# Performance work log

Measured on AMD Instinct MI355X. Metric: run time of the kernel, lower is better.

The kernel has to match this reference:

```python
import jax, jax.numpy as jnp
import numpy as np

N, M, D_IN, HID = 6144, 6144, 16, 256
TEMP = 0.1


def setup_inputs() -> dict:
    key = jax.random.key(0)
    ks = jax.random.split(key, 6)
    sc = lambda k, shape, s: jax.random.normal(k, shape, jnp.float32) * s
    return {
        "q_multivectors": jax.random.normal(ks[0], (N, D_IN), jnp.float32),
        "ret_multivectors": jax.random.normal(ks[1], (M, D_IN), jnp.float32),
        # compressor: LazyLinear(D_IN->HID), GELU, Linear(HID->HID)
        "W1": sc(ks[2], (HID, D_IN), 0.1), "b1": jnp.zeros((HID,), jnp.float32),
        "W2": sc(ks[3], (HID, HID), 0.05), "b2": jnp.zeros((HID,), jnp.float32),
        # nn.Bilinear(HID, HID, 1): weight [1,HID,HID] -> [HID,HID], bias [1] -> scalar
        "Wb": sc(ks[4], (HID, HID), 0.02), "b_bil": jnp.zeros((), jnp.float32),
        "slack_q": jnp.zeros((1,), jnp.float32),
        "slack_ret": jnp.zeros((1,), jnp.float32),
    }


def reference(q_multivectors, ret_multivectors, W1, b1, W2, b2, Wb, b_bil, slack_q, slack_ret):
    def compress(x):  # Linear -> exact GELU -> Linear
        return jax.nn.gelu(x @ W1.T + b1, approximate=False) @ W2.T + b2

    h_q = compress(q_multivectors)    # [n, H]
    h_r = compress(ret_multivectors)  # [m, H]

    # Bilinear(h_q_i, h_r_j) as low-rank factorization: (h_q @ Wb) @ h_r^T + bias
    logits = (h_q @ Wb) @ h_r.T + b_bil  # [n, m]
    n, m = logits.shape

    # row softmax with slack column, then drop slack
    with_slack_col = jnp.concatenate([logits, jnp.broadcast_to(slack_q, (n, 1))], axis=1)
    pi_rows = jax.nn.softmax(with_slack_col / TEMP, axis=1)[:, :-1]

    # column softmax with slack row, then drop slack
    with_slack_row = jnp.concatenate([logits, jnp.broadcast_to(slack_ret, (1, m))], axis=0)
    pi_cols = jax.nn.softmax(with_slack_row / TEMP, axis=0)[:-1, :]

    pi_approx = 0.5 * (pi_rows + pi_cols)
    return pi_approx, logits
```

## Files before the change

### kernel.cpp

```cpp
#include <hip/hip_runtime.h>
#include <hip/hip_bf16.h>
#include <math.h>

#define NQ 6144
#define MR 6144
#define DIN 16
#define HID 256
#define INV_T 10.0f

typedef __attribute__((ext_vector_type(4))) float f32x4;
typedef __attribute__((ext_vector_type(8))) short bf16x8;


static __device__ __forceinline__ unsigned short f2bf(float f) {
  __hip_bfloat16 h = __float2bfloat16(f);
  return __builtin_bit_cast(unsigned short, h);
}

static __device__ __forceinline__ void gload16(const void* g, void* l) {
  __builtin_amdgcn_global_load_lds(
      (const __attribute__((address_space(1))) unsigned int*)g,
      (__attribute__((address_space(3))) unsigned int*)l, 16, 0, 0);
}

__global__ __launch_bounds__(256) void k_prep(
    const float* __restrict__ W2, const float* __restrict__ Wb,
    unsigned short* __restrict__ W2bf, unsigned short* __restrict__ Wbt)
{
  const int idx = blockIdx.x * 256 + threadIdx.x;
  W2bf[idx] = f2bf(W2[idx]);
  const int j = idx >> 8, c = idx & 255;
  Wbt[(size_t)c * 256 + j] = f2bf(Wb[idx]);
}

__global__ __launch_bounds__(256) void k_compress(
    const float* __restrict__ q, const float* __restrict__ ret,
    const float* __restrict__ W1, const float* __restrict__ b1,
    const unsigned short* __restrict__ W2bf, const float* __restrict__ b2,
    const unsigned short* __restrict__ Wbt,
    unsigned short* __restrict__ Apk, unsigned short* __restrict__ Bpk)
{
  const int tid = threadIdx.x;
  const bool is_q = blockIdx.x < (NQ / 16);
  const int grp = is_q ? blockIdx.x : blockIdx.x - NQ / 16;
  const int row0 = grp * 16;
  const float* x = is_q ? q : ret;

  __shared__ float xs[16][DIN];
  __shared__ __align__(16) unsigned short tb[16 * 256];
  __shared__ __align__(16) unsigned short hb[16 * 256];

  ((float*)xs)[tid] = x[(size_t)row0 * DIN + tid];
  __syncthreads();

  {
    float w[DIN];
#pragma unroll
    for (int d = 0; d < DIN; ++d) w[d] = W1[tid * DIN + d];
    const float bb = b1[tid];
#pragma unroll
    for (int rr = 0; rr < 16; ++rr) {
      float a = bb;
#pragma unroll
      for (int d = 0; d < DIN; ++d) a += xs[rr][d] * w[d];
      a = 0.5f * a * (1.0f + erff(a * 0.70710678118654752f));
      tb[rr * 256 + (tid ^ ((rr & 7) << 3))] = f2bf(a);
    }
  }
  __syncthreads();

  const int wid = tid >> 6, lane = tid & 63;
  const int l15 = lane & 15;
  const int lk = (lane >> 4) * 8;

  {
    f32x4 acc[4];
#pragma unroll
    for (int ci = 0; ci < 4; ++ci) acc[ci] = (f32x4)0.0f;

    for (int kk = 0; kk < HID; kk += 32) {
      const bf16x8 a = *(const bf16x8*)&tb[l15 * 256 + ((kk + lk) ^ ((l15 & 7) << 3))];
#pragma unroll
      for (int ci = 0; ci < 4; ++ci) {
        const int bc = wid * 64 + ci * 16 + l15;
        const bf16x8 b = *(const bf16x8*)&W2bf[(size_t)bc * HID + kk + lk];
        acc[ci] = __builtin_amdgcn_mfma_f32_16x16x32_bf16(a, b, acc[ci], 0, 0, 0);
      }
    }

#pragma unroll
    for (int ci = 0; ci < 4; ++ci) {
      const int col = wid * 64 + ci * 16 + l15;
      const float bb2 = b2[col];
#pragma unroll
      for (int qq = 0; qq < 4; ++qq) {
        const int row = (lane >> 4) * 4 + qq;
        hb[row * 256 + (col ^ ((row & 7) << 3))] = f2bf(acc[ci][qq] + bb2);
      }
    }
  }
  __syncthreads();

  if (!is_q) {
#pragma unroll
    for (int i = 0; i < 2; ++i) {
      const int u = i * 256 + tid;
      const int kc = u >> 6, lr = (u >> 2) & 15, ks = u & 3;
      const int k = kc * 32 + ks * 8;
      const bf16x8 v = *(const bf16x8*)&hb[lr * 256 + (k ^ ((lr & 7) << 3))];
      *(bf16x8*)&Bpk[(size_t)grp * 4096 + (size_t)u * 8] = v;
    }
    return;
  }

  {
    f32x4 acc[4];
#pragma unroll
    for (int ci = 0; ci < 4; ++ci) acc[ci] = (f32x4)0.0f;

    for (int kk = 0; kk < HID; kk += 32) {
      const bf16x8 a = *(const bf16x8*)&hb[l15 * 256 + ((kk + lk) ^ ((l15 & 7) << 3))];
#pragma unroll
      for (int ci = 0; ci < 4; ++ci) {
        const int bc = wid * 64 + ci * 16 + l15;
        const bf16x8 b = *(const bf16x8*)&Wbt[(size_t)bc * HID + kk + lk];
        acc[ci] = __builtin_amdgcn_mfma_f32_16x16x32_bf16(a, b, acc[ci], 0, 0, 0);
      }
    }

#pragma unroll
    for (int ci = 0; ci < 4; ++ci) {
      const int col = wid * 64 + ci * 16 + l15;
#pragma unroll
      for (int qq = 0; qq < 4; ++qq) {
        const int row = (lane >> 4) * 4 + qq;
        tb[row * 256 + (col ^ ((row & 7) << 3))] = f2bf(acc[ci][qq]);
      }
    }
  }
  __syncthreads();

#pragma unroll
  for (int i = 0; i < 2; ++i) {
    const int u = i * 256 + tid;
    const int kc = u >> 6, lr = (u >> 2) & 15, ks = u & 3;
    const int k = kc * 32 + ks * 8;
    const bf16x8 v = *(const bf16x8*)&tb[lr * 256 + (k ^ ((lr & 7) << 3))];
    *(bf16x8*)&Apk[(size_t)grp * 4096 + (size_t)u * 8] = v;
  }
}

__global__ __launch_bounds__(512, 4) void k_gemm(
    const unsigned short* __restrict__ Apk,
    const unsigned short* __restrict__ Bpk,
    const float* __restrict__ b_bil,
    float* __restrict__ logF,
    float* __restrict__ rowPS,
    float* __restrict__ colPS)
{
  const int tid = threadIdx.x;
  const int wid = tid >> 6, lane = tid & 63;
  const int wr = wid >> 1, wc = wid & 1;

  const int orig = blockIdx.y * 48 + blockIdx.x;
  const int nid = (orig & 7) * 144 + (orig >> 3);
  const int brow = (nid / 48) * 256;
  const int bcol = (nid % 48) * 128;
  const int brow16 = brow >> 4, bcol16 = bcol >> 4;

  __shared__ __align__(16) unsigned short As[2][8192];
  __shared__ __align__(16) unsigned short Bs[2][4096];

  const int l15 = lane & 15;
  const int ksg = lane >> 4;

  f32x4 acc[4][4];
#pragma unroll
  for (int i = 0; i < 4; ++i)
#pragma unroll
    for (int j = 0; j < 4; ++j) acc[i][j] = (f32x4)0.0f;

  gload16(Apk + (size_t)(brow16 + 2 * wid) * 4096 + lane * 8,
          &As[0][(2 * wid) * 512]);
  gload16(Apk + (size_t)(brow16 + 2 * wid + 1) * 4096 + lane * 8,
          &As[0][(2 * wid + 1) * 512]);
  gload16(Bpk + (size_t)(bcol16 + wid) * 4096 + lane * 8, &Bs[0][wid * 512]);

  int cur = 0;
  for (int kc = 0; kc < 8; ++kc) {
    __syncthreads();
    if (kc < 7) {
      const int kn = (kc + 1) * 512;
      gload16(Apk + (size_t)(brow16 + 2 * wid) * 4096 + kn + lane * 8,
              &As[cur ^ 1][(2 * wid) * 512]);
      gload16(Apk + (size_t)(brow16 + 2 * wid + 1) * 4096 + kn + lane * 8,
              &As[cur ^ 1][(2 * wid + 1) * 512]);
      gload16(Bpk + (size_t)(bcol16 + wid) * 4096 + kn + lane * 8,
              &Bs[cur ^ 1][wid * 512]);
    }
    const int fo = l15 * 32 + ksg * 8;
    bf16x8 a[4], b[4];
#pragma unroll
    for (int mi = 0; mi < 4; ++mi)
      a[mi] = *(const bf16x8*)&As[cur][(wr * 4 + mi) * 512 + fo];
#pragma unroll
    for (int ni = 0; ni < 4; ++ni)
      b[ni] = *(const bf16x8*)&Bs[cur][(wc * 4 + ni) * 512 + fo];
#pragma unroll
    for (int mi = 0; mi < 4; ++mi)
#pragma unroll
      for (int ni = 0; ni < 4; ++ni)
        acc[mi][ni] = __builtin_amdgcn_mfma_f32_16x16x32_bf16(
            a[mi], b[ni], acc[mi][ni], 0, 0, 0);
    cur ^= 1;
  }

  const float bb = b_bil[0];
#pragma unroll
  for (int mi = 0; mi < 4; ++mi)
#pragma unroll
    for (int ni = 0; ni < 4; ++ni)
#pragma unroll
      for (int qq = 0; qq < 4; ++qq) acc[mi][ni][qq] += bb;

  const int r0 = brow + wr * 64 + ksg * 4;
  const int c0 = bcol + wc * 64 + l15;
#pragma unroll
  for (int mi = 0; mi < 4; ++mi)
#pragma unroll
    for (int qq = 0; qq < 4; ++qq) {
      const int rr = r0 + mi * 16 + qq;
#pragma unroll
      for (int ni = 0; ni < 4; ++ni)
        __builtin_nontemporal_store(acc[mi][ni][qq],
                                    &logF[(size_t)rr * MR + c0 + ni * 16]);
    }

  const int cb = (bcol >> 6) + wc;
  const int rb = (brow >> 6) + wr;
  float csum[4] = {0.0f, 0.0f, 0.0f, 0.0f};
#pragma unroll
  for (int mi = 0; mi < 4; ++mi) {
#pragma unroll
    for (int qq = 0; qq < 4; ++qq) {
      float rsum = 0.0f;
#pragma unroll
      for (int ni = 0; ni < 4; ++ni) {
        const float e = __expf(acc[mi][ni][qq] * INV_T);
        rsum += e;
        csum[ni] += e;
      }
      rsum += __shfl_xor(rsum, 1);
      rsum += __shfl_xor(rsum, 2);
      rsum += __shfl_xor(rsum, 4);
      rsum += __shfl_xor(rsum, 8);
      if (l15 == 0) rowPS[(size_t)cb * NQ + (r0 + mi * 16 + qq)] = rsum;
    }
  }
#pragma unroll
  for (int ni = 0; ni < 4; ++ni) {
    csum[ni] += __shfl_xor(csum[ni], 16);
    csum[ni] += __shfl_xor(csum[ni], 32);
  }
  if (lane < 16) {
#pragma unroll
    for (int ni = 0; ni < 4; ++ni)
      colPS[(size_t)rb * MR + (bcol + wc * 64 + ni * 16 + lane)] = csum[ni];
  }
}

__global__ __launch_bounds__(256) void k_comb(
    const float* __restrict__ rowPS, const float* __restrict__ colPS,
    const float* __restrict__ slack_q, const float* __restrict__ slack_ret,
    float* __restrict__ rowR, float* __restrict__ colR)
{
  const int idx = blockIdx.x * 256 + threadIdx.x;
  const bool is_row = idx < NQ;
  const int i = is_row ? idx : idx - NQ;
  const float* ps = is_row ? rowPS : colPS;

  float s = 0.0f;
  for (int c = 0; c < 96; ++c) s += ps[(size_t)c * NQ + i];
  s += __expf((is_row ? slack_q[0] : slack_ret[0]) * INV_T);

  if (is_row) rowR[i] = 0.5f / s;
  else        colR[i] = 0.5f / s;
}

__global__ __launch_bounds__(256) void k_final(
    const float* __restrict__ logF,
    const float* __restrict__ rowR, const float* __restrict__ colR,
    float* __restrict__ out_pi)
{
  const int row = blockIdx.x / 6;
  const int seg = blockIdx.x % 6;
  const int col = seg * 1024 + threadIdx.x * 4;
  const size_t base = (size_t)row * MR + col;

  const float rinv = rowR[row];
  const f32x4 cv = *(const f32x4*)(colR + col);
  const f32x4 l4 = *(const f32x4*)(logF + base);

  f32x4 o;
  o.x = __expf(l4.x * INV_T) * (rinv + cv.x);
  o.y = __expf(l4.y * INV_T) * (rinv + cv.y);
  o.z = __expf(l4.z * INV_T) * (rinv + cv.z);
  o.w = __expf(l4.w * INV_T) * (rinv + cv.w);
  __builtin_nontemporal_store(o, (f32x4*)(out_pi + base));
}

extern "C" void kernel_launch(void* const* d_in, const int* in_sizes, int n_in,
                              void* d_out, int out_size, void* d_ws, size_t ws_size,
                              hipStream_t stream) {
  const float* q  = (const float*)d_in[0];
  const float* r  = (const float*)d_in[1];
  const float* W1 = (const float*)d_in[2];
  const float* b1 = (const float*)d_in[3];
  const float* W2 = (const float*)d_in[4];
  const float* b2 = (const float*)d_in[5];
  const float* Wb = (const float*)d_in[6];
  const float* bb = (const float*)d_in[7];
  const float* sq = (const float*)d_in[8];
  const float* sr = (const float*)d_in[9];

  float* out_pi = (float*)d_out;
  float* out_lg = out_pi + (size_t)NQ * MR;

  char* w = (char*)d_ws;
  size_t off = 0;
  auto alloc = [&](size_t bytes) {
    void* p = w + off;
    off += (bytes + 255) & ~(size_t)255;
    return p;
  };
  unsigned short* Apk  = (unsigned short*)alloc((size_t)NQ * HID * 2);
  unsigned short* Bpk  = (unsigned short*)alloc((size_t)MR * HID * 2);
  unsigned short* W2bf = (unsigned short*)alloc((size_t)HID * HID * 2);
  unsigned short* Wbt  = (unsigned short*)alloc((size_t)HID * HID * 2);
  float* rowR = (float*)alloc((size_t)NQ * 4);
  float* colR = (float*)alloc((size_t)MR * 4);

  float* rowPS = out_pi + (size_t)0 * 96 * NQ;
  float* colPS = out_pi + (size_t)1 * 96 * NQ;

  k_prep<<<dim3(HID * HID / 256), 256, 0, stream>>>(W2, Wb, W2bf, Wbt);
  k_compress<<<dim3((NQ + MR) / 16), 256, 0, stream>>>(q, r, W1, b1, W2bf, b2,
                                                       Wbt, Apk, Bpk);
  k_gemm<<<dim3(48, 24), 512, 0, stream>>>(Apk, Bpk, bb, out_lg, rowPS, colPS);
  k_comb<<<dim3((NQ + MR) / 256), 256, 0, stream>>>(
      rowPS, colPS, sq, sr, rowR, colR);
  k_final<<<dim3(NQ * 6), 256, 0, stream>>>(out_lg, rowR, colR, out_pi);
}
```

Before: 143.9 us.

## Store bf16 exp values from GEMM and triple-buffer the K loop

The GEMM epilogue now also writes exp(logit/T) as bf16 into a workspace buffer when the workspace is large enough. The final kernel then reads 2-byte values instead of re-reading fp32 logits and recomputing exp, which cuts its read traffic in half. The GEMM main loop also moves from double to triple buffering with explicit vmcnt waits and raw barriers, to overlap loads more deeply. The trade-offs are an extra 75 MB write in the GEMM, more LDS per block, and bf16 rounding of the exp values, which lowers the precision of pi.

Result: slower. 154.0 us (+7.0%).

```diff
diff --git a/kernel.cpp b/kernel.cpp
--- a/kernel.cpp
+++ b/kernel.cpp
@@ -15,6 +15,10 @@
 static __device__ __forceinline__ unsigned short f2bf(float f) {
   __hip_bfloat16 h = __float2bfloat16(f);
   return __builtin_bit_cast(unsigned short, h);
+}
+static __device__ __forceinline__ float bf2f(unsigned short u) {
+  unsigned int x = ((unsigned int)u) << 16;
+  return __builtin_bit_cast(float, x);
 }
 
 static __device__ __forceinline__ void gload16(const void* g, void* l) {
@@ -150,13 +154,15 @@
   }
 }
 
+template <bool WRITE_E>
 __global__ __launch_bounds__(512, 4) void k_gemm(
     const unsigned short* __restrict__ Apk,
     const unsigned short* __restrict__ Bpk,
     const float* __restrict__ b_bil,
     float* __restrict__ logF,
     float* __restrict__ rowPS,
-    float* __restrict__ colPS)
+    float* __restrict__ colPS,
+    unsigned short* __restrict__ Ebuf)
 {
   const int tid = threadIdx.x;
   const int wid = tid >> 6, lane = tid & 63;
@@ -168,8 +174,8 @@
   const int bcol = (nid % 48) * 128;
   const int brow16 = brow >> 4, bcol16 = bcol >> 4;
 
-  __shared__ __align__(16) unsigned short As[2][8192];
-  __shared__ __align__(16) unsigned short Bs[2][4096];
+  __shared__ __align__(16) unsigned short As[3][8192];
+  __shared__ __align__(16) unsigned short Bs[3][4096];
 
   const int l15 = lane & 15;
   const int ksg = lane >> 4;
@@ -180,39 +186,49 @@
 #pragma unroll
     for (int j = 0; j < 4; ++j) acc[i][j] = (f32x4)0.0f;
 
-  gload16(Apk + (size_t)(brow16 + 2 * wid) * 4096 + lane * 8,
-          &As[0][(2 * wid) * 512]);
-  gload16(Apk + (size_t)(brow16 + 2 * wid + 1) * 4096 + lane * 8,
-          &As[0][(2 * wid + 1) * 512]);
-  gload16(Bpk + (size_t)(bcol16 + wid) * 4096 + lane * 8, &Bs[0][wid * 512]);
-
-  int cur = 0;
+  const unsigned short* a0 = Apk + (size_t)(brow16 + 2 * wid) * 4096 + lane * 8;
+  const unsigned short* a1 = a0 + 4096;
+  const unsigned short* b0 = Bpk + (size_t)(bcol16 + wid) * 4096 + lane * 8;
+
+  gload16(a0, &As[0][(2 * wid) * 512]);
+  gload16(a1, &As[0][(2 * wid + 1) * 512]);
+  gload16(b0, &Bs[0][wid * 512]);
+  gload16(a0 + 512, &As[1][(2 * wid) * 512]);
+  gload16(a1 + 512, &As[1][(2 * wid + 1) * 512]);
+  gload16(b0 + 512, &Bs[1][wid * 512]);
+
   for (int kc = 0; kc < 8; ++kc) {
-    __syncthreads();
-    if (kc < 7) {
-      const int kn = (kc + 1) * 512;
-      gload16(Apk + (size_t)(brow16 + 2 * wid) * 4096 + kn + lane * 8,
-              &As[cur ^ 1][(2 * wid) * 512]);
-      gload16(Apk + (size_t)(brow16 + 2 * wid + 1) * 4096 + kn + lane * 8,
-              &As[cur ^ 1][(2 * wid + 1) * 512]);
-      gload16(Bpk + (size_t)(bcol16 + wid) * 4096 + kn + lane * 8,
-              &Bs[cur ^ 1][wid * 512]);
-    }
+    if (kc < 6) {
+      const int kn = (kc + 2) * 512;
+      const int nb = (kc + 2) % 3;
+      gload16(a0 + kn, &As[nb][(2 * wid) * 512]);
+      gload16(a1 + kn, &As[nb][(2 * wid + 1) * 512]);
+      gload16(b0 + kn, &Bs[nb][wid * 512]);
+      asm volatile("s_waitcnt vmcnt(6)" ::: "memory");
+    } else if (kc == 6) {
+      asm volatile("s_waitcnt vmcnt(3)" ::: "memory");
+    } else {
+      asm volatile("s_waitcnt vmcnt(0)" ::: "memory");
+    }
+    __builtin_amdgcn_s_barrier();
+
+    const int cb3 = kc % 3;
     const int fo = l15 * 32 + ksg * 8;
     bf16x8 a[4], b[4];
 #pragma unroll
     for (int mi = 0; mi < 4; ++mi)
-      a[mi] = *(const bf16x8*)&As[cur][(wr * 4 + mi) * 512 + fo];
+      a[mi] = *(const bf16x8*)&As[cb3][(wr * 4 + mi) * 512 + fo];
 #pragma unroll
     for (int ni = 0; ni < 4; ++ni)
-      b[ni] = *(const bf16x8*)&Bs[cur][(wc * 4 + ni) * 512 + fo];
+      b[ni] = *(const bf16x8*)&Bs[cb3][(wc * 4 + ni) * 512 + fo];
 #pragma unroll
     for (int mi = 0; mi < 4; ++mi)
 #pragma unroll
       for (int ni = 0; ni < 4; ++ni)
         acc[mi][ni] = __builtin_amdgcn_mfma_f32_16x16x32_bf16(
             a[mi], b[ni], acc[mi][ni], 0, 0, 0);
-    cur ^= 1;
+
+    __builtin_amdgcn_s_barrier();
   }
 
   const float bb = b_bil[0];
@@ -243,10 +259,14 @@
   for (int mi = 0; mi < 4; ++mi) {
 #pragma unroll
     for (int qq = 0; qq < 4; ++qq) {
+      const int rr = r0 + mi * 16 + qq;
       float rsum = 0.0f;
 #pragma unroll
       for (int ni = 0; ni < 4; ++ni) {
         const float e = __expf(acc[mi][ni][qq] * INV_T);
+        if (WRITE_E)
+          __builtin_nontemporal_store(
+              f2bf(e), &Ebuf[(size_t)rr * MR + c0 + ni * 16]);
         rsum += e;
         csum[ni] += e;
       }
@@ -254,7 +274,7 @@
       rsum += __shfl_xor(rsum, 2);
       rsum += __shfl_xor(rsum, 4);
       rsum += __shfl_xor(rsum, 8);
-      if (l15 == 0) rowPS[(size_t)cb * NQ + (r0 + mi * 16 + qq)] = rsum;
+      if (l15 == 0) rowPS[(size_t)cb * NQ + rr] = rsum;
     }
   }
 #pragma unroll
@@ -285,6 +305,34 @@
 
   if (is_row) rowR[i] = 0.5f / s;
   else        colR[i] = 0.5f / s;
+}
+
+__global__ __launch_bounds__(256) void k_final_e(
+    const unsigned short* __restrict__ Ebuf,
+    const float* __restrict__ rowR, const float* __restrict__ colR,
+    float* __restrict__ out_pi)
+{
+  const int row = blockIdx.x / 3;
+  const int seg = blockIdx.x % 3;
+  const int col = seg * 2048 + threadIdx.x * 8;
+  const size_t base = (size_t)row * MR + col;
+
+  const float rinv = rowR[row];
+  const bf16x8 e8 = *(const bf16x8*)(Ebuf + base);
+  const f32x4 cv0 = *(const f32x4*)(colR + col);
+  const f32x4 cv1 = *(const f32x4*)(colR + col + 4);
+
+  f32x4 o0, o1;
+  o0.x = bf2f((unsigned short)e8[0]) * (rinv + cv0.x);
+  o0.y = bf2f((unsigned short)e8[1]) * (rinv + cv0.y);
+  o0.z = bf2f((unsigned short)e8[2]) * (rinv + cv0.z);
+  o0.w = bf2f((unsigned short)e8[3]) * (rinv + cv0.w);
+  o1.x = bf2f((unsigned short)e8[4]) * (rinv + cv1.x);
+  o1.y = bf2f((unsigned short)e8[5]) * (rinv + cv1.y);
+  o1.z = bf2f((unsigned short)e8[6]) * (rinv + cv1.z);
+  o1.w = bf2f((unsigned short)e8[7]) * (rinv + cv1.w);
+  __builtin_nontemporal_store(o0, (f32x4*)(out_pi + base));
+  __builtin_nontemporal_store(o1, (f32x4*)(out_pi + base + 4));
 }
 
 __global__ __launch_bounds__(256) void k_final(
@@ -340,14 +388,27 @@
   float* rowR = (float*)alloc((size_t)NQ * 4);
   float* colR = (float*)alloc((size_t)MR * 4);
 
+  unsigned short* Ebuf = nullptr;
+  if (ws_size >= off + (size_t)NQ * MR * 2 + 1024)
+    Ebuf = (unsigned short*)alloc((size_t)NQ * MR * 2);
+
   float* rowPS = out_pi + (size_t)0 * 96 * NQ;
   float* colPS = out_pi + (size_t)1 * 96 * NQ;
 
   k_prep<<<dim3(HID * HID / 256), 256, 0, stream>>>(W2, Wb, W2bf, Wbt);
   k_compress<<<dim3((NQ + MR) / 16), 256, 0, stream>>>(q, r, W1, b1, W2bf, b2,
                                                        Wbt, Apk, Bpk);
-  k_gemm<<<dim3(48, 24), 512, 0, stream>>>(Apk, Bpk, bb, out_lg, rowPS, colPS);
-  k_comb<<<dim3((NQ + MR) / 256), 256, 0, stream>>>(
-      rowPS, colPS, sq, sr, rowR, colR);
-  k_final<<<dim3(NQ * 6), 256, 0, stream>>>(out_lg, rowR, colR, out_pi);
-}
+  if (Ebuf) {
+    k_gemm<true><<<dim3(48, 24), 512, 0, stream>>>(
+        Apk, Bpk, bb, out_lg, rowPS, colPS, Ebuf);
+    k_comb<<<dim3((NQ + MR) / 256), 256, 0, stream>>>(
+        rowPS, colPS, sq, sr, rowR, colR);
+    k_final_e<<<dim3(NQ * 3), 256, 0, stream>>>(Ebuf, rowR, colR, out_pi);
+  } else {
+    k_gemm<false><<<dim3(48, 24), 512, 0, stream>>>(
+        Apk, Bpk, bb, out_lg, rowPS, colPS, nullptr);
+    k_comb<<<dim3((NQ + MR) / 256), 256, 0, stream>>>(
+        rowPS, colPS, sq, sr, rowR, colR);
+    k_final<<<dim3(NQ * 6), 256, 0, stream>>>(out_lg, rowR, colR, out_pi);
+  }
+}
```
